# Optimization experiments

Hardware: AMD Instinct MI355X
Metric: run time of the kernel (lower is better)

The kernel has to match this reference:

```python
import jax, jax.numpy as jnp
import numpy as np

TOP_K = 20  # MemoryBank top_k default in eval path (softmax_w_top)


def setup_inputs() -> dict:
    key = jax.random.key(0)
    k1, k2, k3, k4 = jax.random.split(key, 4)
    B, CK, CV = 2, 64, 256
    NM, NQ = 32768, 4096  # memory entries (8 frames x 64x64), query entries (64x64)
    return {
        "mk": jax.random.normal(k1, (B, CK, NM), dtype=jnp.float32),
        "qk": jax.random.normal(k2, (B, CK, NQ), dtype=jnp.float32),
        "mv0": jax.random.normal(k3, (B, CV, NM), dtype=jnp.float32),
        "mv1": jax.random.normal(k4, (B, CV, NM), dtype=jnp.float32),
    }


def reference(mk, qk, mv0, mv1):
    # mk: [B, CK, NM], qk: [B, CK, NQ], mv*: [B, CV, NM]
    B, CK, NM = mk.shape
    NQ = qk.shape[-1]
    # affinity = (-||mk||^2 + 2*mk^T qk) / sqrt(CK)   (negative-L2 + dot score)
    a = jnp.sum(mk * mk, axis=1)                        # [B, NM]
    b = 2.0 * jnp.einsum('bcm,bcq->bmq', mk, qk)        # [B, NM, NQ]
    aff = (b - a[:, :, None]) / jnp.sqrt(jnp.asarray(CK, mk.dtype))
    # top-k softmax over the memory dim, scattered back to a sparse dense matrix
    aff_t = jnp.swapaxes(aff, 1, 2)                     # [B, NQ, NM]
    vals, idx = jax.lax.top_k(aff_t, TOP_K)             # [B, NQ, K]
    w = jax.nn.softmax(vals, axis=-1)
    bi = jnp.arange(B)[:, None, None]
    qi = jnp.arange(NQ)[None, :, None]
    sparse = jnp.zeros_like(aff_t).at[bi, qi, idx].set(w)
    affinity = jnp.swapaxes(sparse, 1, 2)               # [B, NM, NQ]
    # per-value bmm readout sharing one affinity
    r0 = jnp.einsum('bcm,bmq->bcq', mv0, affinity)      # [B, CV, NQ]
    r1 = jnp.einsum('bcm,bmq->bcq', mv1, affinity)
    return (r0, r1)
```

## Files before the change

kernel.cpp:

```cpp
#include <hip/hip_runtime.h>
#include <hip/hip_bf16.h>
#include <cstdint>

#define B_  2
#define CK_ 64
#define NM_ 32768
#define NQ_ 4096
#define CV_ 256
#define K_  20
#define SEG2_ 8
#define PARTS_ 16
#define CHUNKS_ 128

typedef unsigned short ushort_t;
typedef unsigned int uint_t;
typedef unsigned long long u64_t;
typedef float f32x4 __attribute__((ext_vector_type(4)));
typedef float f32x16 __attribute__((ext_vector_type(16)));
typedef short short8v __attribute__((ext_vector_type(8)));

__device__ __forceinline__ ushort_t f2bf_rn(float f) {
  uint_t x = __float_as_uint(f);
  uint_t r = x + 0x7FFFu + ((x >> 16) & 1u);
  return (ushort_t)(r >> 16);
}
__device__ __forceinline__ float bf2f(ushort_t u) {
  return __uint_as_float(((uint_t)u) << 16);
}

__global__ __launch_bounds__(256) void prep_mk(const float* __restrict__ mk,
                                               ushort_t* __restrict__ mkt,
                                               ushort_t* __restrict__ mlt,
                                               float* __restrict__ ans) {
  int i = blockIdx.x * 256 + threadIdx.x;
  int b = i >> 15, m = i & (NM_ - 1);
  const float* src = mk + (size_t)b * CK_ * NM_ + m;
  const size_t chbase = ((size_t)(b * 1024 + (m >> 5)) << 11);
  const int ml = m & 31;
  float s = 0.f;
  #pragma unroll
  for (int c8 = 0; c8 < 8; ++c8) {
    ushort_t hh[8], ll[8];
    #pragma unroll
    for (int j = 0; j < 8; ++j) {
      float v = src[(size_t)(c8 * 8 + j) * NM_];
      s = fmaf(v, v, s);
      ushort_t h = f2bf_rn(v);
      hh[j] = h;
      ll[j] = f2bf_rn(v - bf2f(h));
    }
    size_t off = chbase + (c8 << 8) + (ml << 3);
    *reinterpret_cast<short8v*>(mkt + off) = *reinterpret_cast<short8v*>(hh);
    *reinterpret_cast<short8v*>(mlt + off) = *reinterpret_cast<short8v*>(ll);
  }
  ans[i] = 0.125f * s;
}

__global__ __launch_bounds__(256) void prep_qk(const float* __restrict__ qk,
                                               ushort_t* __restrict__ qkh,
                                               ushort_t* __restrict__ qkl) {
  int i = blockIdx.x * 256 + threadIdx.x;
  int b = i >> 12, q = i & (NQ_ - 1);
  const float* src = qk + (size_t)b * CK_ * NQ_ + q;
  ushort_t* dh = qkh + (size_t)i * CK_;
  ushort_t* dl = qkl + (size_t)i * CK_;
  #pragma unroll
  for (int c8 = 0; c8 < 8; ++c8) {
    ushort_t hh[8], ll[8];
    #pragma unroll
    for (int j = 0; j < 8; ++j) {
      float v = 0.25f * src[(size_t)(c8 * 8 + j) * NQ_];
      ushort_t h = f2bf_rn(v);
      hh[j] = h;
      ll[j] = f2bf_rn(v - bf2f(h));
    }
    *reinterpret_cast<short8v*>(dh + c8 * 8) = *reinterpret_cast<short8v*>(hh);
    *reinterpret_cast<short8v*>(dl + c8 * 8) = *reinterpret_cast<short8v*>(ll);
  }
}

__global__ __launch_bounds__(256) void transpose_mv(const float* __restrict__ mv0,
                                                    const float* __restrict__ mv1,
                                                    ushort_t* __restrict__ mvt0,
                                                    ushort_t* __restrict__ mvt1) {
  __shared__ float tl[64][33];
  const int zz = blockIdx.z;
  const int bank = zz & 1, b = zz >> 1;
  const float* src = (bank ? mv1 : mv0) + (size_t)b * CV_ * NM_;
  ushort_t*    dst = (bank ? mvt1 : mvt0) + (size_t)b * NM_ * CV_;
  const int m0 = blockIdx.x * 32, c0 = blockIdx.y * 64;
  const int t = threadIdx.x;
  #pragma unroll
  for (int i = 0; i < 8; ++i) {
    int f = t + 256 * i;
    int c = f >> 5, ml = f & 31;
    tl[c][ml] = src[(size_t)(c0 + c) * NM_ + m0 + ml];
  }
  __syncthreads();
  int m = t >> 3, c8 = t & 7;
  ushort_t pack[8];
  #pragma unroll
  for (int j = 0; j < 8; ++j) pack[j] = f2bf_rn(tl[c8 * 8 + j][m]);
  *reinterpret_cast<short8v*>(dst + (size_t)(m0 + m) * CV_ + c0 + c8 * 8) =
      *reinterpret_cast<short8v*>(pack);
}

#define TKF_FOR(F) F(0) F(1) F(2) F(3) F(4) F(5) F(6) F(7) F(8) F(9) F(10) F(11) F(12) F(13) F(14) F(15) F(16) F(17) F(18) F(19)
#define TKF_DECL(J) float tv##J = -3.4e38f; int ti##J = 0;

#define TKF_SW(A,B) { bool c_ = tv##B > tv##A; \
  float fx_ = fmaxf(tv##A, tv##B); float fn_ = fminf(tv##A, tv##B); \
  int ix_ = c_ ? ti##B : ti##A;    int in_ = c_ ? ti##A : ti##B; \
  tv##A = fx_; tv##B = fn_; ti##A = ix_; ti##B = in_; }

#define TKF_INS(S,M) { if ((S) > tv19) { tv19 = (S); ti19 = (M); \
  TKF_SW(18,19) TKF_SW(17,18) TKF_SW(16,17) TKF_SW(15,16) TKF_SW(14,15) \
  TKF_SW(13,14) TKF_SW(12,13) TKF_SW(11,12) TKF_SW(10,11) TKF_SW(9,10) \
  TKF_SW(8,9) TKF_SW(7,8) TKF_SW(6,7) TKF_SW(5,6) TKF_SW(4,5) \
  TKF_SW(3,4) TKF_SW(2,3) TKF_SW(1,2) TKF_SW(0,1) } }

#define TKF_PUSH(S,M) { float s_ = (S); if (s_ > tv19) { \
  caf5 = caf4; cam5 = cam4; caf4 = caf3; cam4 = cam3; caf3 = caf2; cam3 = cam2; \
  caf2 = caf1; cam2 = cam1; caf1 = caf0; cam1 = cam0; caf0 = s_; cam0 = (M); ++cnt; } }

#define TKD_ONE(J) { float sd_ = (cnt > (J)) ? caf##J : -3.4e38f; int md_ = cam##J; TKF_INS(sd_, md_) }
#define TKF_DRAIN() { TKD_ONE(0) TKD_ONE(1) TKD_ONE(2) TKD_ONE(3) TKD_ONE(4) TKD_ONE(5) cnt = 0; }
#define TKF_CHK() { if (__any(cnt >= 3)) { TKF_DRAIN() } }

#define MFMA32(A,B,C) __builtin_amdgcn_mfma_f32_32x32x16_bf16((A),(B),(C),0,0,0)

#define GLOAD_LDS16(G, L) __builtin_amdgcn_global_load_lds( \
    (__attribute__((address_space(1))) unsigned int*)(G), \
    (__attribute__((address_space(3))) unsigned int*)(L), 16, 0, 0)

__global__ __launch_bounds__(256, 2) void score_topk_mfma(
    const ushort_t* __restrict__ mkt, const ushort_t* __restrict__ mlt,
    const ushort_t* __restrict__ qkh, const ushort_t* __restrict__ qkl,
    const float* __restrict__ ans,
    float* __restrict__ pvals, int* __restrict__ pidx) {
  __shared__ __attribute__((aligned(16))) ushort_t ldsH[2 * 2048];
  __shared__ __attribute__((aligned(16))) ushort_t ldsL[2 * 2048];
  __shared__ __attribute__((aligned(16))) float    ldsA[2 * 32];
  const int t = threadIdx.x;
  const int b = blockIdx.z, seg = blockIdx.y, qblk = blockIdx.x;
  const int w = t >> 6, l = t & 63;
  const int lq = l & 31, hi = l >> 5;
  const int q = qblk * 128 + w * 32 + lq;
  const int gch0 = seg * CHUNKS_;

  const size_t qbase = (((size_t)b * NQ_ + q) << 6) + hi * 8;
  const short8v bh0 = *(const short8v*)(qkh + qbase);
  const short8v bh1 = *(const short8v*)(qkh + qbase + 16);
  const short8v bh2 = *(const short8v*)(qkh + qbase + 32);
  const short8v bh3 = *(const short8v*)(qkh + qbase + 48);
  const short8v bl0 = *(const short8v*)(qkl + qbase);
  const short8v bl1 = *(const short8v*)(qkl + qbase + 16);
  const short8v bl2 = *(const short8v*)(qkl + qbase + 32);
  const short8v bl3 = *(const short8v*)(qkl + qbase + 48);

  TKF_FOR(TKF_DECL)
  float caf0 = 0, caf1 = 0, caf2 = 0, caf3 = 0, caf4 = 0, caf5 = 0;
  int cam0 = 0, cam1 = 0, cam2 = 0, cam3 = 0, cam4 = 0, cam5 = 0;
  int cnt = 0;

#define STAGE(NBUF, GCH) { \
  const size_t cb_ = ((size_t)(b * 1024) + (GCH)) << 11; \
  GLOAD_LDS16(mkt + cb_ + (((w << 6) + l) << 3), &ldsH[(NBUF) * 2048 + (w << 9)]); \
  GLOAD_LDS16(mlt + cb_ + (((w << 6) + l) << 3), &ldsL[(NBUF) * 2048 + (w << 9)]); \
  if (t < 8) GLOAD_LDS16(ans + ((size_t)b << 15) + ((GCH) << 5) + (t << 2), &ldsA[(NBUF) * 32]); \
}

#define ITER(CH, BUF) { \
  int chn_ = (CH) + 1; if (chn_ > CHUNKS_ - 1) chn_ = CHUNKS_ - 1; \
  STAGE(1 - (BUF), gch0 + chn_) \
  const int fro_ = (BUF) * 2048 + (hi << 8) + (lq << 3); \
  const short8v ah0 = *(const short8v*)&ldsH[fro_ + 0 * 512]; \
  const short8v ah1 = *(const short8v*)&ldsH[fro_ + 1 * 512]; \
  const short8v ah2 = *(const short8v*)&ldsH[fro_ + 2 * 512]; \
  const short8v ah3 = *(const short8v*)&ldsH[fro_ + 3 * 512]; \
  const short8v al0 = *(const short8v*)&ldsL[fro_ + 0 * 512]; \
  const short8v al1 = *(const short8v*)&ldsL[fro_ + 1 * 512]; \
  const short8v al2 = *(const short8v*)&ldsL[fro_ + 2 * 512]; \
  const short8v al3 = *(const short8v*)&ldsL[fro_ + 3 * 512]; \
  const float* ap_ = &ldsA[(BUF) * 32 + (hi << 2)]; \
  f32x4 an_a = *(const f32x4*)ap_; \
  f32x4 an_b = *(const f32x4*)(ap_ + 8); \
  f32x4 an_c = *(const f32x4*)(ap_ + 16); \
  f32x4 an_d = *(const f32x4*)(ap_ + 24); \
  f32x16 acc; \
  acc[0]  = -an_a[0]; acc[1]  = -an_a[1]; acc[2]  = -an_a[2]; acc[3]  = -an_a[3]; \
  acc[4]  = -an_b[0]; acc[5]  = -an_b[1]; acc[6]  = -an_b[2]; acc[7]  = -an_b[3]; \
  acc[8]  = -an_c[0]; acc[9]  = -an_c[1]; acc[10] = -an_c[2]; acc[11] = -an_c[3]; \
  acc[12] = -an_d[0]; acc[13] = -an_d[1]; acc[14] = -an_d[2]; acc[15] = -an_d[3]; \
  acc = MFMA32(ah0, bh0, acc); \
  acc = MFMA32(ah1, bh1, acc); \
  acc = MFMA32(ah2, bh2, acc); \
  acc = MFMA32(ah3, bh3, acc); \
  acc = MFMA32(ah0, bl0, acc); \
  acc = MFMA32(ah1, bl1, acc); \
  acc = MFMA32(ah2, bl2, acc); \
  acc = MFMA32(ah3, bl3, acc); \
  acc = MFMA32(al0, bh0, acc); \
  acc = MFMA32(al1, bh1, acc); \
  acc = MFMA32(al2, bh2, acc); \
  acc = MFMA32(al3, bh3, acc); \
  const int mb = ((gch0 + (CH)) << 5) + (hi << 2); \
  TKF_PUSH(acc[0], mb + 0)  TKF_PUSH(acc[1], mb + 1)  TKF_PUSH(acc[2], mb + 2)  TKF_PUSH(acc[3], mb + 3)  TKF_CHK() \
  TKF_PUSH(acc[4], mb + 8)  TKF_PUSH(acc[5], mb + 9)  TKF_PUSH(acc[6], mb + 10) TKF_PUSH(acc[7], mb + 11) TKF_CHK() \
  TKF_PUSH(acc[8], mb + 16) TKF_PUSH(acc[9], mb + 17) TKF_PUSH(acc[10],mb + 18) TKF_PUSH(acc[11],mb + 19) TKF_CHK() \
  TKF_PUSH(acc[12],mb + 24) TKF_PUSH(acc[13],mb + 25) TKF_PUSH(acc[14],mb + 26) TKF_PUSH(acc[15],mb + 27) TKF_CHK() \
  __syncthreads(); \
}

  STAGE(0, gch0)
  __syncthreads();

  #pragma clang loop unroll(disable)
  for (int ch2 = 0; ch2 < CHUNKS_ / 2; ++ch2) {
    const int ch = ch2 * 2;
    ITER(ch, 0)
    ITER(ch + 1, 1)
  }
  if (__any(cnt > 0)) { TKF_DRAIN() }

#undef ITER
#undef STAGE

  const int part = (seg << 1) + hi;
  float* pv = pvals + (((size_t)((b * PARTS_ + part) * K_)) << 12) + q;
  int*   pi = pidx  + (((size_t)((b * PARTS_ + part) * K_)) << 12) + q;
#define TKF_STORE(J) { pv[(size_t)(J) << 12] = tv##J; pi[(size_t)(J) << 12] = ti##J; }
  TKF_FOR(TKF_STORE)
#undef TKF_STORE
}

__global__ __launch_bounds__(256) void merge_kernel(const float* __restrict__ pvals,
                                                    const int* __restrict__ pidx,
                                                    float* __restrict__ fw,
                                                    int* __restrict__ fidx, int S) {
  int i = blockIdx.x * 256 + threadIdx.x;
  int b = i >> 12, q = i & (NQ_ - 1);

  float vals[K_]; int idxs[K_];
  #pragma unroll
  for (int j = 0; j < K_; ++j) { vals[j] = -3.4e38f; idxs[j] = 0; }

  for (int seg = 0; seg < S; ++seg) {
    #pragma unroll
    for (int j = 0; j < K_; ++j) {
      size_t o = (size_t)((b * S + seg) * K_ + j) * NQ_ + q;
      float v = pvals[o];
      if (v > vals[K_ - 1]) {
        int m = pidx[o];
        vals[K_ - 1] = v; idxs[K_ - 1] = m;
        #pragma unroll
        for (int jj = K_ - 1; jj > 0; --jj) {
          if (vals[jj] > vals[jj - 1]) {
            float tv = vals[jj]; vals[jj] = vals[jj - 1]; vals[jj - 1] = tv;
            int   ti = idxs[jj]; idxs[jj] = idxs[jj - 1]; idxs[jj - 1] = ti;
          }
        }
      }
    }
  }

  float mx = vals[0];
  float w[K_]; float sum = 0.f;
  #pragma unroll
  for (int j = 0; j < K_; ++j) { w[j] = expf(vals[j] - mx); sum += w[j]; }
  float inv = 1.f / sum;
  #pragma unroll
  for (int j = 0; j < K_; ++j) {
    size_t o = (size_t)(b * K_ + j) * NQ_ + q;
    fw[o] = w[j] * inv; fidx[o] = idxs[j];
  }
}

__global__ __launch_bounds__(256) void readout_bf16(const ushort_t* __restrict__ mvt0,
                                                    const ushort_t* __restrict__ mvt1,
                                                    const float* __restrict__ fw,
                                                    const int* __restrict__ fidx,
                                                    float* __restrict__ out) {
  __shared__ float mw[16][K_];
  __shared__ int   mi[16][K_];
  __shared__ float ob0[256][17];
  __shared__ float ob1[256][17];
  const int t = threadIdx.x;
  const int b = blockIdx.y;
  const int q0 = blockIdx.x * 16;

  for (int i = t; i < 16 * K_; i += 256) {
    int qp = i / K_, k = i % K_;
    size_t o = (size_t)(b * K_ + k) * NQ_ + q0 + qp;
    mw[qp][k] = fw[o];
    mi[qp][k] = fidx[o];
  }
  __syncthreads();

  const int c2 = (t & 127) * 2, hq = t >> 7;
  for (int qp = hq * 8; qp < hq * 8 + 8; ++qp) {
    float a00 = 0.f, a01 = 0.f, a10 = 0.f, a11 = 0.f;
    #pragma unroll 5
    for (int k = 0; k < K_; ++k) {
      int m = mi[qp][k]; float ww = mw[qp][k];
      size_t o = ((size_t)(b * NM_ + m) << 8) + c2;
      uint_t v0 = *reinterpret_cast<const uint_t*>(mvt0 + o);
      uint_t v1 = *reinterpret_cast<const uint_t*>(mvt1 + o);
      a00 = fmaf(ww, __uint_as_float(v0 << 16), a00);
      a01 = fmaf(ww, __uint_as_float(v0 & 0xFFFF0000u), a01);
      a10 = fmaf(ww, __uint_as_float(v1 << 16), a10);
      a11 = fmaf(ww, __uint_as_float(v1 & 0xFFFF0000u), a11);
    }
    ob0[c2][qp] = a00; ob0[c2 + 1][qp] = a01;
    ob1[c2][qp] = a10; ob1[c2 + 1][qp] = a11;
  }
  __syncthreads();

  float* out0 = out + (size_t)b * CV_ * NQ_;
  float* out1 = out + (size_t)B_ * CV_ * NQ_ + (size_t)b * CV_ * NQ_;
  for (int i = t; i < 256 * 16; i += 256) {
    int c = i >> 4, qp = i & 15;
    out0[(size_t)c * NQ_ + q0 + qp] = ob0[c][qp];
    out1[(size_t)c * NQ_ + q0 + qp] = ob1[c][qp];
  }
}

__global__ __launch_bounds__(256) void readout_f32(const float* __restrict__ v0src,
                                                   const float* __restrict__ v1src,
                                                   const float* __restrict__ fw,
                                                   const int* __restrict__ fidx,
                                                   float* __restrict__ out) {
  __shared__ float mw[16][K_];
  __shared__ int   mi[16][K_];
  __shared__ float ob0[256][17];
  __shared__ float ob1[256][17];
  const int t = threadIdx.x;
  const int b = blockIdx.y;
  const int q0 = blockIdx.x * 16;

  for (int i = t; i < 16 * K_; i += 256) {
    int qp = i / K_, k = i % K_;
    size_t o = (size_t)(b * K_ + k) * NQ_ + q0 + qp;
    mw[qp][k] = fw[o];
    mi[qp][k] = fidx[o];
  }
  __syncthreads();

  for (int qp = 0; qp < 16; ++qp) {
    float a0 = 0.f, a1 = 0.f;
    #pragma unroll 5
    for (int k = 0; k < K_; ++k) {
      int m = mi[qp][k]; float ww = mw[qp][k];
      size_t o = (size_t)b * CV_ * NM_ + (size_t)t * NM_ + m;
      a0 = fmaf(ww, v0src[o], a0);
      a1 = fmaf(ww, v1src[o], a1);
    }
    ob0[t][qp] = a0; ob1[t][qp] = a1;
  }
  __syncthreads();

  float* out0 = out + (size_t)b * CV_ * NQ_;
  float* out1 = out + (size_t)B_ * CV_ * NQ_ + (size_t)b * CV_ * NQ_;
  for (int i = t; i < 256 * 16; i += 256) {
    int c = i >> 4, qp = i & 15;
    out0[(size_t)c * NQ_ + q0 + qp] = ob0[c][qp];
    out1[(size_t)c * NQ_ + q0 + qp] = ob1[c][qp];
  }
}

extern "C" void kernel_launch(void* const* d_in, const int* in_sizes, int n_in,
                              void* d_out, int out_size, void* d_ws, size_t ws_size,
                              hipStream_t stream) {
  (void)in_sizes; (void)n_in; (void)out_size;
  const float* mk  = (const float*)d_in[0];
  const float* qk  = (const float*)d_in[1];
  const float* mv0 = (const float*)d_in[2];
  const float* mv1 = (const float*)d_in[3];
  float* out = (float*)d_out;

  auto al = [](size_t x) { return (x + 255) & ~(size_t)255; };
  const size_t mkB  = (size_t)B_ * NM_ * CK_ * 2;
  const size_t qkB  = (size_t)B_ * NQ_ * CK_ * 2;
  const size_t anB  = (size_t)B_ * NM_ * 4;
  const size_t prtB = (size_t)B_ * PARTS_ * K_ * NQ_ * 4;
  const size_t finB = (size_t)B_ * K_ * NQ_ * 4;
  const size_t tpB  = (size_t)B_ * NM_ * CV_ * 2;

  const size_t core = 2 * al(mkB) + 2 * al(qkB) + al(anB) + 2 * al(prtB) + 2 * al(finB);
  const bool tp = ws_size >= core + 2 * al(tpB);

  char* p = (char*)d_ws;
  ushort_t* mkt = (ushort_t*)p; p += al(mkB);
  ushort_t* mlt = (ushort_t*)p; p += al(mkB);
  ushort_t* qkh = (ushort_t*)p; p += al(qkB);
  ushort_t* qkl = (ushort_t*)p; p += al(qkB);
  float* ans    = (float*)p;    p += al(anB);
  float* pvals  = (float*)p;    p += al(prtB);
  int*   pidx   = (int*)p;      p += al(prtB);
  float* fw     = (float*)p;    p += al(finB);
  int*   fidx   = (int*)p;      p += al(finB);
  ushort_t* mvt0 = nullptr, * mvt1 = nullptr;
  if (tp) { mvt0 = (ushort_t*)p; p += al(tpB); mvt1 = (ushort_t*)p; p += al(tpB); }

  prep_mk<<<B_ * NM_ / 256, 256, 0, stream>>>(mk, mkt, mlt, ans);
  prep_qk<<<B_ * NQ_ / 256, 256, 0, stream>>>(qk, qkh, qkl);
  if (tp)
    transpose_mv<<<dim3(NM_ / 32, CV_ / 64, B_ * 2), 256, 0, stream>>>(mv0, mv1, mvt0, mvt1);
  score_topk_mfma<<<dim3(NQ_ / 128, SEG2_, B_), 256, 0, stream>>>(mkt, mlt, qkh, qkl, ans, pvals, pidx);
  merge_kernel<<<B_ * NQ_ / 256, 256, 0, stream>>>(pvals, pidx, fw, fidx, PARTS_);
  if (tp) readout_bf16<<<dim3(NQ_ / 16, B_), 256, 0, stream>>>(mvt0, mvt1, fw, fidx, out);
  else    readout_f32<<<dim3(NQ_ / 16, B_), 256, 0, stream>>>(mv0, mv1, fw, fidx, out);
}
```

Measured before the change: 600.1 us.

## Double segment count for score/top-k, add warm-up insert and early-exit merge

Picks the number of memory segments for the score/top-k kernel at runtime from the workspace size, doubling it to 16 when space allows so the grid has more blocks per device. The first chunk of each block now inserts directly into the top-k list without the buffered push path. The sign of the norm term moves into the prep kernel so the accumulator is initialised with a plain copy. The merge kernel gains a wave-uniform early break once no lane can improve its list. The trade-off is more partial results to write and merge, and a runtime-variable loop bound.

```diff
diff --git a/kernel.cpp b/kernel.cpp
--- a/kernel.cpp
+++ b/kernel.cpp
@@ -8,9 +8,6 @@
 #define NQ_ 4096
 #define CV_ 256
 #define K_  20
-#define SEG2_ 8
-#define PARTS_ 16
-#define CHUNKS_ 128
 
 typedef unsigned short ushort_t;
 typedef unsigned int uint_t;
@@ -53,7 +50,7 @@
     *reinterpret_cast<short8v*>(mkt + off) = *reinterpret_cast<short8v*>(hh);
     *reinterpret_cast<short8v*>(mlt + off) = *reinterpret_cast<short8v*>(ll);
   }
-  ans[i] = 0.125f * s;
+  ans[i] = -0.125f * s;
 }
 
 __global__ __launch_bounds__(256) void prep_qk(const float* __restrict__ qk,
@@ -143,10 +140,12 @@
   __shared__ __attribute__((aligned(16))) float    ldsA[2 * 32];
   const int t = threadIdx.x;
   const int b = blockIdx.z, seg = blockIdx.y, qblk = blockIdx.x;
+  const int segcnt = gridDim.y;
+  const int chunks = (NM_ / 32) / segcnt;
   const int w = t >> 6, l = t & 63;
   const int lq = l & 31, hi = l >> 5;
   const int q = qblk * 128 + w * 32 + lq;
-  const int gch0 = seg * CHUNKS_;
+  const int gch0 = seg * chunks;
 
   const size_t qbase = (((size_t)b * NQ_ + q) << 6) + hi * 8;
   const short8v bh0 = *(const short8v*)(qkh + qbase);
@@ -170,8 +169,8 @@
   if (t < 8) GLOAD_LDS16(ans + ((size_t)b << 15) + ((GCH) << 5) + (t << 2), &ldsA[(NBUF) * 32]); \
 }
 
-#define ITER(CH, BUF) { \
-  int chn_ = (CH) + 1; if (chn_ > CHUNKS_ - 1) chn_ = CHUNKS_ - 1; \
+#define COMPUTE(CH, BUF) \
+  int chn_ = (CH) + 1; if (chn_ > chunks - 1) chn_ = chunks - 1; \
   STAGE(1 - (BUF), gch0 + chn_) \
   const int fro_ = (BUF) * 2048 + (hi << 8) + (lq << 3); \
   const short8v ah0 = *(const short8v*)&ldsH[fro_ + 0 * 512]; \
@@ -188,10 +187,10 @@
   f32x4 an_c = *(const f32x4*)(ap_ + 16); \
   f32x4 an_d = *(const f32x4*)(ap_ + 24); \
   f32x16 acc; \
-  acc[0]  = -an_a[0]; acc[1]  = -an_a[1]; acc[2]  = -an_a[2]; acc[3]  = -an_a[3]; \
-  acc[4]  = -an_b[0]; acc[5]  = -an_b[1]; acc[6]  = -an_b[2]; acc[7]  = -an_b[3]; \
-  acc[8]  = -an_c[0]; acc[9]  = -an_c[1]; acc[10] = -an_c[2]; acc[11] = -an_c[3]; \
-  acc[12] = -an_d[0]; acc[13] = -an_d[1]; acc[14] = -an_d[2]; acc[15] = -an_d[3]; \
+  acc[0]  = an_a[0]; acc[1]  = an_a[1]; acc[2]  = an_a[2]; acc[3]  = an_a[3]; \
+  acc[4]  = an_b[0]; acc[5]  = an_b[1]; acc[6]  = an_b[2]; acc[7]  = an_b[3]; \
+  acc[8]  = an_c[0]; acc[9]  = an_c[1]; acc[10] = an_c[2]; acc[11] = an_c[3]; \
+  acc[12] = an_d[0]; acc[13] = an_d[1]; acc[14] = an_d[2]; acc[15] = an_d[3]; \
   acc = MFMA32(ah0, bh0, acc); \
   acc = MFMA32(ah1, bh1, acc); \
   acc = MFMA32(ah2, bh2, acc); \
@@ -204,7 +203,10 @@
   acc = MFMA32(al1, bh1, acc); \
   acc = MFMA32(al2, bh2, acc); \
   acc = MFMA32(al3, bh3, acc); \
-  const int mb = ((gch0 + (CH)) << 5) + (hi << 2); \
+  const int mb = ((gch0 + (CH)) << 5) + (hi << 2);
+
+#define ITER(CH, BUF) { \
+  COMPUTE(CH, BUF) \
   TKF_PUSH(acc[0], mb + 0)  TKF_PUSH(acc[1], mb + 1)  TKF_PUSH(acc[2], mb + 2)  TKF_PUSH(acc[3], mb + 3)  TKF_CHK() \
   TKF_PUSH(acc[4], mb + 8)  TKF_PUSH(acc[5], mb + 9)  TKF_PUSH(acc[6], mb + 10) TKF_PUSH(acc[7], mb + 11) TKF_CHK() \
   TKF_PUSH(acc[8], mb + 16) TKF_PUSH(acc[9], mb + 17) TKF_PUSH(acc[10],mb + 18) TKF_PUSH(acc[11],mb + 19) TKF_CHK() \
@@ -212,11 +214,22 @@
   __syncthreads(); \
 }
 
+#define ITER_WARM(CH, BUF) { \
+  COMPUTE(CH, BUF) \
+  TKF_INS(acc[0], mb + 0)  TKF_INS(acc[1], mb + 1)  TKF_INS(acc[2], mb + 2)  TKF_INS(acc[3], mb + 3)  \
+  TKF_INS(acc[4], mb + 8)  TKF_INS(acc[5], mb + 9)  TKF_INS(acc[6], mb + 10) TKF_INS(acc[7], mb + 11) \
+  TKF_INS(acc[8], mb + 16) TKF_INS(acc[9], mb + 17) TKF_INS(acc[10],mb + 18) TKF_INS(acc[11],mb + 19) \
+  TKF_INS(acc[12],mb + 24) TKF_INS(acc[13],mb + 25) TKF_INS(acc[14],mb + 26) TKF_INS(acc[15],mb + 27) \
+  __syncthreads(); \
+}
+
   STAGE(0, gch0)
   __syncthreads();
 
+  ITER_WARM(0, 0)
+  ITER(1, 1)
   #pragma clang loop unroll(disable)
-  for (int ch2 = 0; ch2 < CHUNKS_ / 2; ++ch2) {
+  for (int ch2 = 1; ch2 < chunks / 2; ++ch2) {
     const int ch = ch2 * 2;
     ITER(ch, 0)
     ITER(ch + 1, 1)
@@ -224,11 +237,14 @@
   if (__any(cnt > 0)) { TKF_DRAIN() }
 
 #undef ITER
+#undef ITER_WARM
+#undef COMPUTE
 #undef STAGE
 
   const int part = (seg << 1) + hi;
-  float* pv = pvals + (((size_t)((b * PARTS_ + part) * K_)) << 12) + q;
-  int*   pi = pidx  + (((size_t)((b * PARTS_ + part) * K_)) << 12) + q;
+  const int parts = segcnt << 1;
+  float* pv = pvals + (((size_t)((b * parts + part) * K_)) << 12) + q;
+  int*   pi = pidx  + (((size_t)((b * parts + part) * K_)) << 12) + q;
 #define TKF_STORE(J) { pv[(size_t)(J) << 12] = tv##J; pi[(size_t)(J) << 12] = ti##J; }
   TKF_FOR(TKF_STORE)
 #undef TKF_STORE
@@ -246,12 +262,14 @@
   for (int j = 0; j < K_; ++j) { vals[j] = -3.4e38f; idxs[j] = 0; }
 
   for (int seg = 0; seg < S; ++seg) {
-    #pragma unroll
+    const float* pp = pvals + (((size_t)((b * S + seg) * K_)) << 12) + q;
+    const int*   qq = pidx  + (((size_t)((b * S + seg) * K_)) << 12) + q;
+    #pragma clang loop unroll(disable)
     for (int j = 0; j < K_; ++j) {
-      size_t o = (size_t)((b * S + seg) * K_ + j) * NQ_ + q;
-      float v = pvals[o];
+      float v = pp[(size_t)j << 12];
+      if (__all(v <= vals[K_ - 1])) break;
       if (v > vals[K_ - 1]) {
-        int m = pidx[o];
+        int m = qq[(size_t)j << 12];
         vals[K_ - 1] = v; idxs[K_ - 1] = m;
         #pragma unroll
         for (int jj = K_ - 1; jj > 0; --jj) {
@@ -382,12 +400,19 @@
   const size_t mkB  = (size_t)B_ * NM_ * CK_ * 2;
   const size_t qkB  = (size_t)B_ * NQ_ * CK_ * 2;
   const size_t anB  = (size_t)B_ * NM_ * 4;
-  const size_t prtB = (size_t)B_ * PARTS_ * K_ * NQ_ * 4;
   const size_t finB = (size_t)B_ * K_ * NQ_ * 4;
   const size_t tpB  = (size_t)B_ * NM_ * CV_ * 2;
-
-  const size_t core = 2 * al(mkB) + 2 * al(qkB) + al(anB) + 2 * al(prtB) + 2 * al(finB);
-  const bool tp = ws_size >= core + 2 * al(tpB);
+  auto prtB = [](int parts) { return (size_t)B_ * parts * K_ * NQ_ * 4; };
+  auto core = [&](int parts) {
+    return 2 * al(mkB) + 2 * al(qkB) + al(anB) + 2 * al(prtB(parts)) + 2 * al(finB);
+  };
+
+  int segcnt; bool tp;
+  if      (ws_size >= core(32) + 2 * al(tpB)) { segcnt = 16; tp = true;  }
+  else if (ws_size >= core(16) + 2 * al(tpB)) { segcnt = 8;  tp = true;  }
+  else if (ws_size >= core(16))               { segcnt = 8;  tp = false; }
+  else                                        { segcnt = 4;  tp = false; }
+  const int parts = segcnt * 2;
 
   char* p = (char*)d_ws;
   ushort_t* mkt = (ushort_t*)p; p += al(mkB);
@@ -395,8 +420,8 @@
   ushort_t* qkh = (ushort_t*)p; p += al(qkB);
   ushort_t* qkl = (ushort_t*)p; p += al(qkB);
   float* ans    = (float*)p;    p += al(anB);
-  float* pvals  = (float*)p;    p += al(prtB);
-  int*   pidx   = (int*)p;      p += al(prtB);
+  float* pvals  = (float*)p;    p += al(prtB(parts));
+  int*   pidx   = (int*)p;      p += al(prtB(parts));
   float* fw     = (float*)p;    p += al(finB);
   int*   fidx   = (int*)p;      p += al(finB);
   ushort_t* mvt0 = nullptr, * mvt1 = nullptr;
@@ -406,8 +431,8 @@
   prep_qk<<<B_ * NQ_ / 256, 256, 0, stream>>>(qk, qkh, qkl);
   if (tp)
     transpose_mv<<<dim3(NM_ / 32, CV_ / 64, B_ * 2), 256, 0, stream>>>(mv0, mv1, mvt0, mvt1);
-  score_topk_mfma<<<dim3(NQ_ / 128, SEG2_, B_), 256, 0, stream>>>(mkt, mlt, qkh, qkl, ans, pvals, pidx);
-  merge_kernel<<<B_ * NQ_ / 256, 256, 0, stream>>>(pvals, pidx, fw, fidx, PARTS_);
+  score_topk_mfma<<<dim3(NQ_ / 128, segcnt, B_), 256, 0, stream>>>(mkt, mlt, qkh, qkl, ans, pvals, pidx);
+  merge_kernel<<<B_ * NQ_ / 256, 256, 0, stream>>>(pvals, pidx, fw, fidx, parts);
   if (tp) readout_bf16<<<dim3(NQ_ / 16, B_), 256, 0, stream>>>(mvt0, mvt1, fw, fidx, out);
   else    readout_f32<<<dim3(NQ_ / 16, B_), 256, 0, stream>>>(mv0, mv1, fw, fidx, out);
 }
```

Measured after the change: 666.2 us. +11.0%, slower.
